# Performance work log

Measured on AMD Instinct MI355X. Metric: run time of the kernel, lower is better.

## Reference

```python
import jax, jax.numpy as jnp
import numpy as np

EMBED_DIM = 768
NUM_HEADS = 12


def setup_inputs() -> dict:
    key = jax.random.key(0)
    ks = jax.random.split(key, 9)
    B, N, C = 16, 1024, EMBED_DIM
    std = 1.0 / np.sqrt(C)
    x = jax.random.normal(ks[0], (B, N, C), dtype=jnp.float32)
    def w(k):
        return jax.random.normal(k, (C, C), dtype=jnp.float32) * std
    def b(k):
        return jax.random.normal(k, (C,), dtype=jnp.float32) * 0.01
    return {
        "x": x,
        "Wq": w(ks[1]), "bq": b(ks[2]),
        "Wk": w(ks[3]), "bk": b(ks[4]),
        "Wv": w(ks[5]), "bv": b(ks[6]),
        "Wo": w(ks[7]), "bo": b(ks[8]),
    }


def reference(x, Wq, bq, Wk, bk, Wv, bv, Wo, bo):
    B, N, C = x.shape
    H = NUM_HEADS
    Dh = C // H
    scale = 1.0 / np.sqrt(Dh)

    q = x @ Wq + bq  # (B, N, C)
    k = x @ Wk + bk
    v = x @ Wv + bv

    # Faithful to the original: (B, N, H, Dh) -> reshape(B*H, N, Dh)
    # WITHOUT transposing, exactly as torch_mla_core does (row-major reshape).
    q2 = q.reshape(B * H, N, Dh)
    k2 = k.reshape(B * H, N, Dh)
    v2 = v.reshape(B * H, N, Dh)

    scores = jnp.einsum('gld,gmd->glm', q2, k2) * scale  # (B*H, N, N)
    attn = jax.nn.softmax(scores, axis=-1)
    ctx2 = jnp.einsum('glm,gmd->gld', attn, v2)  # (B*H, N, Dh)

    ctx = ctx2.reshape(B, H, N, Dh).transpose(0, 2, 1, 3).reshape(B, N, C)
    out = ctx @ Wo + bo
    return out
```

## Files before the change

kernel.cpp:

```cpp
#include <hip/hip_runtime.h>
#include <hip/hip_bf16.h>
#include <cstdint>
#include <cstddef>

typedef unsigned short u16;
typedef __attribute__((ext_vector_type(8))) short s8v;
typedef __attribute__((ext_vector_type(4))) float f4v;
typedef __attribute__((ext_vector_type(8))) u16 u16x8;
typedef __attribute__((ext_vector_type(4))) uint32_t u32x4;

#define AS1 __attribute__((address_space(1)))
#define AS3 __attribute__((address_space(3)))

#define BATCH 16
#define SEQ   1024
#define EMBED 768
#define HEADS 12
#define DH    64
#define MTOT  (BATCH*SEQ)

__device__ __forceinline__ u16 f2bf(float f) {
    union { float f; uint32_t u; } v; v.f = f;
    uint32_t r = v.u + 0x7fffu + ((v.u >> 16) & 1u);
    return (u16)(r >> 16);
}

__device__ __forceinline__ void gll16(const u16* g, u16* l) {
    __builtin_amdgcn_global_load_lds((AS1 void*)g, (AS3 void*)l, 16, 0, 0);
}

#define XBLOCKS 12288
__global__ void k_pack(const float* __restrict__ x, u16* __restrict__ xb, int nx,
                       const float* __restrict__ Wq, const float* __restrict__ Wk,
                       const float* __restrict__ Wv, const float* __restrict__ Wo,
                       const float* __restrict__ bq, const float* __restrict__ bk,
                       const float* __restrict__ bv,
                       u16* __restrict__ wqkvT, u16* __restrict__ woT,
                       float* __restrict__ bqkv)
{
    if (blockIdx.x < XBLOCKS) {
        int i = (blockIdx.x * 256 + threadIdx.x) * 4;
        if (i + 3 < nx) {
            float4 f = *(const float4*)(x + i);
            ushort4 o;
            o.x = f2bf(f.x); o.y = f2bf(f.y); o.z = f2bf(f.z); o.w = f2bf(f.w);
            *(ushort4*)(xb + i) = o;
        }
        return;
    }
    const int NQKV = 2304 * 768;
    const int NO = 768 * 768;
    int t = (blockIdx.x - XBLOCKS) * 256 + threadIdx.x;
    if (t < NQKV) {
        int n = t % 2304, k = t / 2304;
        const float* src; int nn; float sc;
        if (n < 768)       { src = Wq; nn = n;        sc = 0.125f; }
        else if (n < 1536) { src = Wk; nn = n - 768;  sc = 1.0f;   }
        else               { src = Wv; nn = n - 1536; sc = 1.0f;   }
        wqkvT[(size_t)n * 768 + k] = f2bf(src[(size_t)k * 768 + nn] * sc);
    } else if (t < NQKV + NO) {
        int t2 = t - NQKV;
        int n = t2 % 768, k = t2 / 768;
        woT[(size_t)n * 768 + k] = f2bf(Wo[(size_t)k * 768 + n]);
    } else if (t < NQKV + NO + 2304) {
        int t3 = t - NQKV - NO;
        bqkv[t3] = (t3 < 768) ? bq[t3] * 0.125f
                 : ((t3 < 1536) ? bk[t3 - 768] : bv[t3 - 1536]);
    }
}

template<int MODE>
__global__ __launch_bounds__(256) void k_gemm(
    const u16* __restrict__ A, const u16* __restrict__ BT,
    const float* __restrict__ bias,
    u16* __restrict__ oq, u16* __restrict__ okk, u16* __restrict__ ov,
    float* __restrict__ of)
{
    __shared__ __attribute__((aligned(16))) u16 As[128 * 32];
    __shared__ __attribute__((aligned(16))) u16 Bs[128 * 32];
    const int tid = threadIdx.x;
    const int m0 = blockIdx.x * 128;
    const int n0 = blockIdx.y * 128;
    const int wv = tid >> 6;
    const int ln = tid & 63;
    const int l15 = ln & 15, quad = ln >> 4;
    const int wm = (wv >> 1) * 64, wn = (wv & 1) * 64;
    const int r = tid >> 2, c8 = (tid & 3) * 8;

    const u16* gA0 = A + (size_t)(m0 + r) * 768 + c8;
    const u16* gA1 = gA0 + 64 * 768;
    const u16* gB0 = BT + (size_t)(n0 + r) * 768 + c8;
    const u16* gB1 = gB0 + 64 * 768;
    u16* lA0 = As + wv * 512;
    u16* lA1 = As + 2048 + wv * 512;
    u16* lB0 = Bs + wv * 512;
    u16* lB1 = Bs + 2048 + wv * 512;

    f4v acc[4][4] = {};

    for (int kt = 0; kt < 24; ++kt) {
        const int ko = kt * 32;
        gll16(gA0 + ko, lA0);
        gll16(gA1 + ko, lA1);
        gll16(gB0 + ko, lB0);
        gll16(gB1 + ko, lB1);
        __syncthreads();
        s8v aF[4], bF[4];
#pragma unroll
        for (int i = 0; i < 4; ++i)
            aF[i] = *(const s8v*)(As + (wm + i * 16 + l15) * 32 + quad * 8);
#pragma unroll
        for (int j = 0; j < 4; ++j)
            bF[j] = *(const s8v*)(Bs + (wn + j * 16 + l15) * 32 + quad * 8);
#pragma unroll
        for (int i = 0; i < 4; ++i)
#pragma unroll
            for (int j = 0; j < 4; ++j)
                acc[i][j] = __builtin_amdgcn_mfma_f32_16x16x32_bf16(aF[i], bF[j], acc[i][j], 0, 0, 0);
        __syncthreads();
    }

#pragma unroll
    for (int j = 0; j < 4; ++j) {
        int n = n0 + wn + j * 16 + l15;
        float bs = bias[n];
        if (MODE == 0) {
            u16* dst; int nn;
            if (n < 768)       { dst = oq;  nn = n; }
            else if (n < 1536) { dst = okk; nn = n - 768; }
            else               { dst = ov;  nn = n - 1536; }
#pragma unroll
            for (int i = 0; i < 4; ++i) {
                int mrow = m0 + wm + i * 16 + quad * 4;
#pragma unroll
                for (int rg = 0; rg < 4; ++rg)
                    dst[(size_t)(mrow + rg) * 768 + nn] = f2bf(acc[i][j][rg] + bs);
            }
        } else {
#pragma unroll
            for (int i = 0; i < 4; ++i) {
                int mrow = m0 + wm + i * 16 + quad * 4;
#pragma unroll
                for (int rg = 0; rg < 4; ++rg)
                    of[(size_t)(mrow + rg) * 768 + n] = acc[i][j][rg] + bs;
            }
        }
    }
}

__global__ void k_transpose_v(const u16* __restrict__ v, u16* __restrict__ vt) {
    __shared__ __attribute__((aligned(16))) u16 ts[64 * 80];
    int g = blockIdx.x >> 4;
    int l0 = (blockIdx.x & 15) << 6;
    const u16* vg = v + (size_t)g * 65536;
    u16* vtg = vt + (size_t)g * 65536;
    int tid = threadIdx.x;
#pragma unroll
    for (int c = tid; c < 512; c += 256) {
        int l = c >> 3, d0 = (c & 7) * 8;
        *(uint4*)(ts + l * 80 + d0) = *(const uint4*)(vg + (size_t)(l0 + l) * 64 + d0);
    }
    __syncthreads();
#pragma unroll
    for (int c = tid; c < 512; c += 256) {
        int d = c >> 3, lc = (c & 7) * 8;
        u16x8 tv;
#pragma unroll
        for (int i = 0; i < 8; ++i) tv[i] = ts[(lc + i) * 80 + d];
        *(u16x8*)(vtg + (size_t)d * 1024 + l0 + lc) = tv;
    }
}

#define KS2(r_, c_) ( ((r_) << 6) + (((((c_) >> 3) ^ ((r_) & 7)) & 7) << 3) + ((c_) & 7) )

__global__ __launch_bounds__(256) void k_attn(
    const u16* __restrict__ qb, const u16* __restrict__ kb,
    const u16* __restrict__ vt, u16* __restrict__ ctx)
{
    __shared__ __attribute__((aligned(16))) u16 Ks[128 * 64];
    __shared__ __attribute__((aligned(16))) u16 Vts[64 * 136];

    const int g = blockIdx.x >> 4;
    const int q0 = (blockIdx.x & 15) << 6;
    const int tid = threadIdx.x, wv = tid >> 6;
    const int ln = tid & 63, l15 = ln & 15, quad = ln >> 4;
    const u16* qg = qb + (size_t)g * 65536;
    const u16* kg = kb + (size_t)g * 65536;
    const u16* vtg = vt + (size_t)g * 65536;

    const u16* qrow = qg + (size_t)(q0 + wv * 16 + l15) * 64 + quad * 8;
    s8v aQ0 = *(const s8v*)qrow;
    s8v aQ1 = *(const s8v*)(qrow + 32);

    const int krr = tid >> 3, kcb = (tid & 7) * 8;
    const int vd = tid >> 4, vc0 = (tid & 15) * 8;
    const u16* kgp = kg + (size_t)krr * 64 + kcb;
    const u16* vgp = vtg + (size_t)vd * 1024 + vc0;

    f4v o[4] = {};
    float rsum = 0.f;

    for (int jt = 0; jt < 8; ++jt) {
        __syncthreads();
        {
            const size_t koff = (size_t)jt * 8192;
            const int voff = jt * 128;
            uint4 kv0 = *(const uint4*)(kgp + koff);
            uint4 kv1 = *(const uint4*)(kgp + koff + 2048);
            uint4 kv2 = *(const uint4*)(kgp + koff + 4096);
            uint4 kv3 = *(const uint4*)(kgp + koff + 6144);
            uint4 vv0 = *(const uint4*)(vgp + voff);
            uint4 vv1 = *(const uint4*)(vgp + voff + 16384);
            uint4 vv2 = *(const uint4*)(vgp + voff + 32768);
            uint4 vv3 = *(const uint4*)(vgp + voff + 49152);
            *(uint4*)(Ks + KS2(krr,      kcb)) = kv0;
            *(uint4*)(Ks + KS2(krr + 32, kcb)) = kv1;
            *(uint4*)(Ks + KS2(krr + 64, kcb)) = kv2;
            *(uint4*)(Ks + KS2(krr + 96, kcb)) = kv3;
            *(uint4*)(Vts + (vd     ) * 136 + vc0) = vv0;
            *(uint4*)(Vts + (vd + 16) * 136 + vc0) = vv1;
            *(uint4*)(Vts + (vd + 32) * 136 + vc0) = vv2;
            *(uint4*)(Vts + (vd + 48) * 136 + vc0) = vv3;
        }
        __syncthreads();

        f4v s[8];
        __builtin_amdgcn_s_setprio(1);
#pragma unroll
        for (int ns = 0; ns < 8; ++ns) {
            int rK = ns * 16 + l15;
            s8v b0 = *(const s8v*)(Ks + KS2(rK, quad * 8));
            s8v b1 = *(const s8v*)(Ks + KS2(rK, quad * 8 + 32));
            f4v t = {};
            t = __builtin_amdgcn_mfma_f32_16x16x32_bf16(b0, aQ0, t, 0, 0, 0);
            t = __builtin_amdgcn_mfma_f32_16x16x32_bf16(b1, aQ1, t, 0, 0, 0);
            s[ns] = t;
        }
        __builtin_amdgcn_s_setprio(0);

#pragma unroll
        for (int ns = 0; ns < 8; ++ns)
#pragma unroll
            for (int rg = 0; rg < 4; ++rg) {
                float p = __expf(s[ns][rg]);
                s[ns][rg] = p;
                rsum += p;
            }

        __builtin_amdgcn_s_setprio(1);
#pragma unroll
        for (int ks = 0; ks < 4; ++ks) {
            uint32_t a0, a1, c0, c1;
            asm("v_cvt_pk_bf16_f32 %0, %1, %2" : "=v"(a0) : "v"(s[2*ks][0]),   "v"(s[2*ks][1]));
            asm("v_cvt_pk_bf16_f32 %0, %1, %2" : "=v"(a1) : "v"(s[2*ks][2]),   "v"(s[2*ks][3]));
            asm("v_cvt_pk_bf16_f32 %0, %1, %2" : "=v"(c0) : "v"(s[2*ks+1][0]), "v"(s[2*ks+1][1]));
            asm("v_cvt_pk_bf16_f32 %0, %1, %2" : "=v"(c1) : "v"(s[2*ks+1][2]), "v"(s[2*ks+1][3]));
            asm("v_permlane32_swap_b32 %0, %1" : "+v"(a0), "+v"(c0));
            asm("v_permlane16_swap_b32 %0, %1" : "+v"(a0), "+v"(c0));
            asm("v_permlane32_swap_b32 %0, %1" : "+v"(a1), "+v"(c1));
            asm("v_permlane16_swap_b32 %0, %1" : "+v"(a1), "+v"(c1));
            u32x4 pk; pk.x = a0; pk.y = a1; pk.z = c0; pk.w = c1;
            s8v aP = __builtin_bit_cast(s8v, pk);
#pragma unroll
            for (int ds = 0; ds < 4; ++ds) {
                s8v bV = *(const s8v*)(Vts + (ds * 16 + l15) * 136 + ks * 32 + quad * 8);
                o[ds] = __builtin_amdgcn_mfma_f32_16x16x32_bf16(aP, bV, o[ds], 0, 0, 0);
            }
        }
        __builtin_amdgcn_s_setprio(0);
    }

    rsum += __shfl_xor(rsum, 16, 64);
    rsum += __shfl_xor(rsum, 32, 64);

    const int b = g / 12, h = g % 12;
    u16* cbase = ctx + (size_t)b * 786432 + h * 64;
#pragma unroll
    for (int rg = 0; rg < 4; ++rg) {
        float rs = __shfl(rsum, 20 * quad + rg, 64);
        float inv = 1.0f / rs;
        int row = q0 + wv * 16 + quad * 4 + rg;
#pragma unroll
        for (int ds = 0; ds < 4; ++ds)
            cbase[(size_t)row * 768 + ds * 16 + l15] = f2bf(o[ds][rg] * inv);
    }
}

extern "C" void kernel_launch(void* const* d_in, const int* in_sizes, int n_in,
                              void* d_out, int out_size, void* d_ws, size_t ws_size,
                              hipStream_t stream) {
    const float* x  = (const float*)d_in[0];
    const float* Wq = (const float*)d_in[1];
    const float* bq = (const float*)d_in[2];
    const float* Wk = (const float*)d_in[3];
    const float* bk = (const float*)d_in[4];
    const float* Wv = (const float*)d_in[5];
    const float* bv = (const float*)d_in[6];
    const float* Wo = (const float*)d_in[7];
    const float* bo = (const float*)d_in[8];
    float* out = (float*)d_out;

    const size_t NTOK = (size_t)MTOT * EMBED;
    char* w = (char*)d_ws;
    u16* xb    = (u16*)w;              w += NTOK * 2;
    u16* qb    = (u16*)w;              w += NTOK * 2;
    u16* kb    = (u16*)w;              w += NTOK * 2;
    u16* vb    = (u16*)w;              w += NTOK * 2;
    u16* vtb   = (u16*)w;              w += NTOK * 2;
    u16* wqkvT = (u16*)w;              w += (size_t)2304 * 768 * 2;
    u16* woT   = (u16*)w;              w += (size_t)768 * 768 * 2;
    float* bqkv = (float*)w;           w += 2304 * 4;
    u16* ctx = xb;

    k_pack<<<XBLOCKS + 9225, 256, 0, stream>>>(x, xb, (int)NTOK,
        Wq, Wk, Wv, Wo, bq, bk, bv, wqkvT, woT, bqkv);

    dim3 g1(128, 18);
    k_gemm<0><<<g1, 256, 0, stream>>>(xb, wqkvT, bqkv, qb, kb, vb, nullptr);

    k_transpose_v<<<3072, 256, 0, stream>>>(vb, vtb);
    k_attn<<<3072, 256, 0, stream>>>(qb, kb, vtb, ctx);

    dim3 g2(128, 6);
    k_gemm<1><<<g2, 256, 0, stream>>>(ctx, woT, bo, nullptr, nullptr, nullptr, out);
}
```

Baseline: 337.9 us.

## Replace projection GEMMs with 256x256 double-buffered swizzled-LDS 8-wave kernel

Rewrites the QKV and output projection GEMMs to use 256x256 block tiles with 8 waves, K-step 64, double-buffered LDS with XOR swizzle, and staged prefetch interleaved with MFMA phases plus an XCD-aware block remap. The aim is more data reuse per LDS load, overlap of global loads with compute, and fewer bank conflicts. The cost is 128 KB of LDS per block, which limits occupancy, and the output GEMM launches only 192 blocks, which may underfill the GPU.

```diff
diff --git a/kernel.cpp b/kernel.cpp
--- a/kernel.cpp
+++ b/kernel.cpp
@@ -69,60 +69,97 @@
     }
 }
 
+#define NT 12
+
 template<int MODE>
-__global__ __launch_bounds__(256) void k_gemm(
+__global__ __launch_bounds__(512, 2) void k_gemm8(
     const u16* __restrict__ A, const u16* __restrict__ BT,
     const float* __restrict__ bias,
     u16* __restrict__ oq, u16* __restrict__ okk, u16* __restrict__ ov,
-    float* __restrict__ of)
+    float* __restrict__ of, int NBN)
 {
-    __shared__ __attribute__((aligned(16))) u16 As[128 * 32];
-    __shared__ __attribute__((aligned(16))) u16 Bs[128 * 32];
-    const int tid = threadIdx.x;
-    const int m0 = blockIdx.x * 128;
-    const int n0 = blockIdx.y * 128;
-    const int wv = tid >> 6;
-    const int ln = tid & 63;
-    const int l15 = ln & 15, quad = ln >> 4;
-    const int wm = (wv >> 1) * 64, wn = (wv & 1) * 64;
-    const int r = tid >> 2, c8 = (tid & 3) * 8;
-
-    const u16* gA0 = A + (size_t)(m0 + r) * 768 + c8;
-    const u16* gA1 = gA0 + 64 * 768;
-    const u16* gB0 = BT + (size_t)(n0 + r) * 768 + c8;
-    const u16* gB1 = gB0 + 64 * 768;
-    u16* lA0 = As + wv * 512;
-    u16* lA1 = As + 2048 + wv * 512;
-    u16* lB0 = Bs + wv * 512;
-    u16* lB1 = Bs + 2048 + wv * 512;
-
-    f4v acc[4][4] = {};
-
-    for (int kt = 0; kt < 24; ++kt) {
-        const int ko = kt * 32;
-        gll16(gA0 + ko, lA0);
-        gll16(gA1 + ko, lA1);
-        gll16(gB0 + ko, lB0);
-        gll16(gB1 + ko, lB1);
-        __syncthreads();
-        s8v aF[4], bF[4];
-#pragma unroll
-        for (int i = 0; i < 4; ++i)
-            aF[i] = *(const s8v*)(As + (wm + i * 16 + l15) * 32 + quad * 8);
-#pragma unroll
-        for (int j = 0; j < 4; ++j)
-            bF[j] = *(const s8v*)(Bs + (wn + j * 16 + l15) * 32 + quad * 8);
-#pragma unroll
-        for (int i = 0; i < 4; ++i)
-#pragma unroll
-            for (int j = 0; j < 4; ++j)
-                acc[i][j] = __builtin_amdgcn_mfma_f32_16x16x32_bf16(aF[i], bF[j], acc[i][j], 0, 0, 0);
-        __syncthreads();
-    }
-
-#pragma unroll
-    for (int j = 0; j < 4; ++j) {
-        int n = n0 + wn + j * 16 + l15;
+    __shared__ __attribute__((aligned(16))) u16 AB[2][16384];
+    __shared__ __attribute__((aligned(16))) u16 BB[2][16384];
+
+    const int nwg = gridDim.x;
+    const int bid = blockIdx.x;
+    const int wg = (bid & 7) * (nwg >> 3) + (bid >> 3);
+    const int bm = wg / NBN, bn = wg % NBN;
+    const int m0 = bm * 256, n0 = bn * 256;
+
+    const int tid = threadIdx.x, wv = tid >> 6;
+    const int ln = tid & 63, l15 = ln & 15, quad = ln >> 4;
+    const int wm = wv >> 2, wn = wv & 3;
+
+    const int chnk = ((tid & 7) ^ ((tid >> 3) & 7)) * 8;
+    const u16* pA = A + (size_t)(m0 + (tid >> 3)) * 768 + chnk;
+    const u16* pB = BT + (size_t)(n0 + (tid >> 8) * 64 + ((tid >> 3) & 31)) * 768 + chnk;
+
+#define STG_A(BUF, mh, kt) { \
+    const u16* s_ = pA + (mh) * 49152 + (kt) * 64; \
+    gll16(s_,          (BUF) + (mh) * 8192 + wv * 512); \
+    gll16(s_ + 98304,  (BUF) + (mh) * 8192 + 4096 + wv * 512); }
+#define STG_B(BUF, nh, kt) { \
+    const u16* s_ = pB + (nh) * 24576 + (kt) * 64; \
+    gll16(s_,          (BUF) + (nh) * 8192 + wv * 512); \
+    gll16(s_ + 98304,  (BUF) + (nh) * 8192 + 4096 + wv * 512); }
+
+    const int offA = wm * 4096 + l15 * 64;
+    const int offB = wn * 2048 + l15 * 64;
+    const int ph0 = ((quad)     ^ (l15 & 7)) * 8;
+    const int ph1 = ((4 + quad) ^ (l15 & 7)) * 8;
+
+    f4v acc[8][4] = {};
+
+    STG_A(&AB[0][0], 0, 0); STG_B(&BB[0][0], 0, 0);
+    STG_A(&AB[0][0], 1, 0); STG_B(&BB[0][0], 1, 0);
+    STG_A(&AB[1][0], 0, 1); STG_B(&BB[1][0], 0, 1);
+
+#define PHASE(mh, nh, STAGE) { \
+    s8v a_[4][2], b_[2][2]; \
+    _Pragma("unroll") \
+    for (int i = 0; i < 4; ++i) { \
+        a_[i][0] = *(const s8v*)(Acur + offA + (mh) * 8192 + i * 1024 + ph0); \
+        a_[i][1] = *(const s8v*)(Acur + offA + (mh) * 8192 + i * 1024 + ph1); } \
+    _Pragma("unroll") \
+    for (int j = 0; j < 2; ++j) { \
+        b_[j][0] = *(const s8v*)(Bcur + offB + (nh) * 8192 + j * 1024 + ph0); \
+        b_[j][1] = *(const s8v*)(Bcur + offB + (nh) * 8192 + j * 1024 + ph1); } \
+    STAGE; \
+    __builtin_amdgcn_s_barrier(); \
+    __builtin_amdgcn_s_setprio(1); \
+    _Pragma("unroll") \
+    for (int i = 0; i < 4; ++i) \
+    _Pragma("unroll") \
+    for (int j = 0; j < 2; ++j) { \
+        acc[(mh)*4+i][(nh)*2+j] = __builtin_amdgcn_mfma_f32_16x16x32_bf16(a_[i][0], b_[j][0], acc[(mh)*4+i][(nh)*2+j], 0, 0, 0); \
+        acc[(mh)*4+i][(nh)*2+j] = __builtin_amdgcn_mfma_f32_16x16x32_bf16(a_[i][1], b_[j][1], acc[(mh)*4+i][(nh)*2+j], 0, 0, 0); } \
+    __builtin_amdgcn_s_setprio(0); \
+    __builtin_amdgcn_s_barrier(); }
+
+    for (int s = 0; s < NT; ++s) {
+        const int cur = s & 1;
+        u16* Acur = &AB[cur][0];
+        u16* Bcur = &BB[cur][0];
+        u16* Anxt = &AB[cur ^ 1][0];
+        u16* Bnxt = &BB[cur ^ 1][0];
+
+        if (s == NT - 1) { asm volatile("s_waitcnt vmcnt(0)" ::: "memory"); }
+        else             { asm volatile("s_waitcnt vmcnt(4)" ::: "memory"); }
+        __builtin_amdgcn_s_barrier();
+
+        PHASE(0, 0, if (s < NT - 1) STG_A(Anxt, 1, s + 1));
+        PHASE(0, 1, if (s < NT - 1) STG_B(Bnxt, 1, s + 1));
+        PHASE(1, 0, if (s < NT - 2) STG_A(Acur, 0, s + 2));
+        PHASE(1, 1, if (s < NT - 2) STG_B(Bcur, 0, s + 2));
+    }
+#undef PHASE
+#undef STG_A
+#undef STG_B
+
+#pragma unroll
+    for (int jg = 0; jg < 4; ++jg) {
+        int n = n0 + wn * 64 + jg * 16 + l15;
         float bs = bias[n];
         if (MODE == 0) {
             u16* dst; int nn;
@@ -130,19 +167,19 @@
             else if (n < 1536) { dst = okk; nn = n - 768; }
             else               { dst = ov;  nn = n - 1536; }
 #pragma unroll
-            for (int i = 0; i < 4; ++i) {
-                int mrow = m0 + wm + i * 16 + quad * 4;
+            for (int ig = 0; ig < 8; ++ig) {
+                int mrow = m0 + wm * 128 + ig * 16 + quad * 4;
 #pragma unroll
                 for (int rg = 0; rg < 4; ++rg)
-                    dst[(size_t)(mrow + rg) * 768 + nn] = f2bf(acc[i][j][rg] + bs);
+                    dst[(size_t)(mrow + rg) * 768 + nn] = f2bf(acc[ig][jg][rg] + bs);
             }
         } else {
 #pragma unroll
-            for (int i = 0; i < 4; ++i) {
-                int mrow = m0 + wm + i * 16 + quad * 4;
+            for (int ig = 0; ig < 8; ++ig) {
+                int mrow = m0 + wm * 128 + ig * 16 + quad * 4;
 #pragma unroll
                 for (int rg = 0; rg < 4; ++rg)
-                    of[(size_t)(mrow + rg) * 768 + n] = acc[i][j][rg] + bs;
+                    of[(size_t)(mrow + rg) * 768 + n] = acc[ig][jg][rg] + bs;
             }
         }
     }
@@ -315,12 +352,10 @@
     k_pack<<<XBLOCKS + 9225, 256, 0, stream>>>(x, xb, (int)NTOK,
         Wq, Wk, Wv, Wo, bq, bk, bv, wqkvT, woT, bqkv);
 
-    dim3 g1(128, 18);
-    k_gemm<0><<<g1, 256, 0, stream>>>(xb, wqkvT, bqkv, qb, kb, vb, nullptr);
+    k_gemm8<0><<<576, 512, 0, stream>>>(xb, wqkvT, bqkv, qb, kb, vb, nullptr, 9);
 
     k_transpose_v<<<3072, 256, 0, stream>>>(vb, vtb);
     k_attn<<<3072, 256, 0, stream>>>(qb, kb, vtb, ctx);
 
-    dim3 g2(128, 6);
-    k_gemm<1><<<g2, 256, 0, stream>>>(ctx, woT, bo, nullptr, nullptr, nullptr, out);
-}
+    k_gemm8<1><<<192, 512, 0, stream>>>(ctx, woT, bo, nullptr, nullptr, nullptr, out, 3);
+}
```

After: 364.1 us. 7.8% more time.
